# Optimization experiments

Measured on AMD Instinct MI355X. Metric: run time of the kernel, lower is better.

## Reference

```python
import jax, jax.numpy as jnp
import numpy as np

N_EMB = 1024
HEAD_SIZE = 128

def setup_inputs() -> dict:
    key = jax.random.key(0)
    kx, kq, kk, kv = jax.random.split(key, 4)
    s = 1.0 / np.sqrt(N_EMB)
    return {
        "x": jax.random.normal(kx, (4, 4096, N_EMB), dtype=jnp.float32),
        "Wq": jax.random.normal(kq, (N_EMB, HEAD_SIZE), dtype=jnp.float32) * s,
        "Wk": jax.random.normal(kk, (N_EMB, HEAD_SIZE), dtype=jnp.float32) * s,
        "Wv": jax.random.normal(kv, (N_EMB, HEAD_SIZE), dtype=jnp.float32) * s,
    }

def reference(x, Wq, Wk, Wv) -> jnp.ndarray:
    B, T, C = x.shape
    q = jnp.einsum('btc,cd->btd', x, Wq)  # [B,T,H]
    k = jnp.einsum('btc,cd->btd', x, Wk)
    v = jnp.einsum('btc,cd->btd', x, Wv)
    # NOTE: original scales by sqrt(n_emb), not sqrt(head_size)
    wei = jnp.einsum('btd,bsd->bts', q, k) / jnp.sqrt(jnp.asarray(C, x.dtype))
    causal = jnp.tril(jnp.ones((T, T), dtype=bool))
    wei = jnp.where(causal, wei, -jnp.inf)
    wei = jax.nn.softmax(wei, axis=-1)
    return jnp.einsum('bts,bsd->btd', wei, v)
```

## Files before the change

### kernel.cpp

```cpp
#include <hip/hip_runtime.h>
#include <hip/hip_bf16.h>


#define TSEQ 4096
#define NBATCH 4
#define CEMB 1024
#define HS 128
#define NWORK 144

typedef float  f32x4  __attribute__((ext_vector_type(4)));
typedef float  f32x16 __attribute__((ext_vector_type(16)));
typedef __bf16 bf16x4 __attribute__((ext_vector_type(4)));
typedef __bf16 bf16x8 __attribute__((ext_vector_type(8)));

__device__ __forceinline__ __bf16 f2b(float f) { return (__bf16)f; }
__device__ __forceinline__ float fexp2(float f) { return __builtin_amdgcn_exp2f(f); }

__global__ void wtrans_kernel(const float* __restrict__ Wq,
                              const float* __restrict__ Wk,
                              const float* __restrict__ Wv,
                              __bf16* __restrict__ Wt) {
  const float* W = (blockIdx.y == 0) ? Wq : (blockIdx.y == 1) ? Wk : Wv;
  int g  = blockIdx.x * 256 + threadIdx.x;
  int n  = g & 127;
  int k0 = (g >> 7) * 8;
  bf16x8 v;
#pragma unroll
  for (int i = 0; i < 8; ++i) v[i] = f2b(W[(size_t)(k0 + i) * HS + n]);
  *(bf16x8*)(Wt + (size_t)blockIdx.y * HS * CEMB + (size_t)n * CEMB + k0) = v;
}

__global__ __launch_bounds__(256)
void proj_kernel(const float* __restrict__ x, const __bf16* __restrict__ Wt,
                 __bf16* __restrict__ qb, __bf16* __restrict__ kb,
                 __bf16* __restrict__ vt) {
  __shared__ __align__(16) __bf16 As[32 * 64];
  __shared__ __align__(16) __bf16 Bs[128 * 64];

  const int tid  = threadIdx.x;
  const int lane = tid & 63;
  const int w    = tid >> 6;
  const int l31  = lane & 31;
  const int half = lane >> 5;

  const int bid = blockIdx.x;
  const int xcd = bid & 7;
  const int i3  = bid >> 3;
  const int mat = i3 % 3;
  const int mb  = xcd + 8 * (i3 / 3);
  const int m0  = mb * 32;
  const __bf16* Wm = Wt + (size_t)mat * HS * CEMB;

  f32x16 acc;
#pragma unroll
  for (int r = 0; r < 16; ++r) acc[r] = 0.f;

  const int ar = 8 * w + (lane >> 4);
  const int ac = lane & 15;
  const int br = 32 * w + (lane >> 3);
  const int bu = lane & 7;

  for (int ks = 0; ks < CEMB; ks += 64) {
    __syncthreads();
#pragma unroll
    for (int i = 0; i < 2; ++i) {
      int r = ar + 4 * i;
      f32x4 f = *(const f32x4*)(x + (size_t)(m0 + r) * CEMB + ks + ac * 4);
      bf16x4 h;
#pragma unroll
      for (int j = 0; j < 4; ++j) h[j] = f2b(f[j]);
      int u = ac >> 1;
      int up = u ^ (r & 7);
      *(bf16x4*)(As + r * 64 + up * 8 + (ac & 1) * 4) = h;
    }
#pragma unroll
    for (int i = 0; i < 4; ++i) {
      int r = br + 8 * i;
      bf16x8 v = *(const bf16x8*)(Wm + (size_t)r * CEMB + ks + bu * 8);
      int up = bu ^ (r & 7);
      *(bf16x8*)(Bs + r * 64 + up * 8) = v;
    }
    __syncthreads();
#pragma unroll
    for (int kc = 0; kc < 4; ++kc) {
      int ua = (2 * kc + half) ^ (l31 & 7);
      bf16x8 af = *(const bf16x8*)(As + l31 * 64 + ua * 8);
      bf16x8 bf = *(const bf16x8*)(Bs + (32 * w + l31) * 64 + ua * 8);
      acc = __builtin_amdgcn_mfma_f32_32x32x16_bf16(af, bf, acc, 0, 0, 0);
    }
  }

  const int n = 32 * w + l31;
  const float qscale = 1.4426950408889634f / 32.0f;
  if (mat == 0) {
#pragma unroll
    for (int r = 0; r < 16; ++r) {
      int m = m0 + (r & 3) + 8 * (r >> 2) + 4 * half;
      qb[(size_t)m * HS + n] = f2b(acc[r] * qscale);
    }
  } else if (mat == 1) {
#pragma unroll
    for (int r = 0; r < 16; ++r) {
      int m = m0 + (r & 3) + 8 * (r >> 2) + 4 * half;
      kb[(size_t)m * HS + n] = f2b(acc[r]);
    }
  } else {
    const int bt = mb >> 7;
#pragma unroll
    for (int g = 0; g < 4; ++g) {
      bf16x4 pk;
#pragma unroll
      for (int d = 0; d < 4; ++d) pk[d] = f2b(acc[4 * g + d]);
      int tl = (m0 & 4095) + 8 * g + 4 * half;
      *(bf16x4*)(vt + ((size_t)bt * HS + n) * TSEQ + tl) = pk;
    }
  }
}

__global__ __launch_bounds__(256)
void attn_kernel(const __bf16* __restrict__ qb, const __bf16* __restrict__ kb,
                 const __bf16* __restrict__ vt,
                 float* __restrict__ Opart, float* __restrict__ Lpart) {
  __shared__ __align__(16) __bf16 Kt[64 * 136];
  __shared__ __align__(16) __bf16 Vtl[128 * 72];
  __shared__ __align__(16) __bf16 Ptl[4 * 32 * 72];

  const int tid   = threadIdx.x;
  const int lane  = tid & 63;
  const int w     = tid >> 6;
  const int l31   = lane & 31;
  const int half  = lane >> 5;
  const int batch = blockIdx.y;
  const int xw    = NWORK - 1 - blockIdx.x;

  int g = 0;
  while (xw >= 2 * (g + 1) * (g + 2)) ++g;
  const int nsp   = g + 1;
  const int rel   = xw - 2 * g * (g + 1);
  const int qin   = rel / nsp;
  const int split = rel - qin * nsp;
  const int q     = 4 * g + qin;
  const int ntile = 2 * (q + 1);
  const int tps   = (ntile + nsp - 1) / nsp;
  const int it0   = split * tps;
  const int it1   = min(it0 + tps, ntile);

  const int strip0 = q * 128 + w * 32;
  const size_t bbase = (size_t)batch * TSEQ;

  bf16x8 qf[8];
  {
    const __bf16* qr = qb + (bbase + strip0 + l31) * HS + half * 8;
#pragma unroll
    for (int kc = 0; kc < 8; ++kc) qf[kc] = *(const bf16x8*)(qr + kc * 16);
  }

  f32x16 o[4];
#pragma unroll
  for (int nt = 0; nt < 4; ++nt)
#pragma unroll
    for (int r = 0; r < 16; ++r) o[nt][r] = 0.f;
  float lsum[16];
#pragma unroll
  for (int r = 0; r < 16; ++r) lsum[r] = 0.f;

  for (int it = it0; it < it1; ++it) {
    const int c0 = it * 64;
    __syncthreads();
    {
      const __bf16* src = kb + (bbase + c0) * HS;
#pragma unroll
      for (int i = 0; i < 4; ++i) {
        int c = tid + i * 256;
        int row = c >> 4, off = c & 15;
        *(int4*)(&Kt[row * 136 + off * 8]) = *(const int4*)(src + row * HS + off * 8);
      }
      const __bf16* vsrc = vt + (size_t)batch * HS * TSEQ + c0;
#pragma unroll
      for (int i = 0; i < 4; ++i) {
        int c = tid + i * 256;
        int n = c >> 3, off = c & 7;
        *(int4*)(&Vtl[n * 72 + off * 8]) = *(const int4*)(vsrc + (size_t)n * TSEQ + off * 8);
      }
    }
    __syncthreads();

    if (c0 <= strip0 + 31) {
      f32x16 s[2];
#pragma unroll
      for (int t = 0; t < 2; ++t)
#pragma unroll
        for (int r = 0; r < 16; ++r) s[t][r] = 0.f;
#pragma unroll
      for (int t = 0; t < 2; ++t)
#pragma unroll
        for (int kc = 0; kc < 8; ++kc) {
          bf16x8 kf = *(const bf16x8*)(&Kt[(t * 32 + l31) * 136 + kc * 16 + half * 8]);
          s[t] = __builtin_amdgcn_mfma_f32_32x32x16_bf16(qf[kc], kf, s[t], 0, 0, 0);
        }
#pragma unroll
      for (int t = 0; t < 2; ++t) {
        if (c0 + t * 32 + 31 > strip0) {
          int j = c0 + t * 32 + l31;
#pragma unroll
          for (int r = 0; r < 16; ++r) {
            int iloc = 4 * half + (r & 3) + 8 * (r >> 2);
            if (j > strip0 + iloc) s[t][r] = -INFINITY;
          }
        }
      }
#pragma unroll
      for (int r = 0; r < 16; ++r) {
        float p0 = fexp2(s[0][r]);
        float p1 = fexp2(s[1][r]);
        s[0][r] = p0; s[1][r] = p1;
        lsum[r] += p0 + p1;
      }
#pragma unroll
      for (int t = 0; t < 2; ++t)
#pragma unroll
        for (int r = 0; r < 16; ++r) {
          int iloc = 4 * half + (r & 3) + 8 * (r >> 2);
          Ptl[(w * 32 + iloc) * 72 + t * 32 + l31] = f2b(s[t][r]);
        }
      asm volatile("s_waitcnt lgkmcnt(0)" ::: "memory");
      bf16x8 pf[4];
#pragma unroll
      for (int kk = 0; kk < 4; ++kk)
        pf[kk] = *(const bf16x8*)(&Ptl[(w * 32 + l31) * 72 + kk * 16 + half * 8]);
#pragma unroll
      for (int nt = 0; nt < 4; ++nt)
#pragma unroll
        for (int kk = 0; kk < 4; ++kk) {
          bf16x8 vf = *(const bf16x8*)(&Vtl[(nt * 32 + l31) * 72 + kk * 16 + half * 8]);
          o[nt] = __builtin_amdgcn_mfma_f32_32x32x16_bf16(pf[kk], vf, o[nt], 0, 0, 0);
        }
    }
  }

  const size_t widx = (size_t)batch * NWORK + xw;
  float* Op = Opart + widx * (128 * 128);
#pragma unroll
  for (int r = 0; r < 16; ++r) {
    int rloc = w * 32 + 4 * half + (r & 3) + 8 * (r >> 2);
#pragma unroll
    for (int nt = 0; nt < 4; ++nt)
      Op[rloc * 128 + nt * 32 + l31] = o[nt][r];
  }
#pragma unroll
  for (int r = 0; r < 16; ++r) {
    float v = lsum[r];
    v += __shfl_xor(v, 1);
    v += __shfl_xor(v, 2);
    v += __shfl_xor(v, 4);
    v += __shfl_xor(v, 8);
    v += __shfl_xor(v, 16);
    lsum[r] = v;
  }
  if (l31 == 0) {
#pragma unroll
    for (int r = 0; r < 16; ++r) {
      int rloc = w * 32 + 4 * half + (r & 3) + 8 * (r >> 2);
      Lpart[widx * 128 + rloc] = lsum[r];
    }
  }
}

__global__ __launch_bounds__(256)
void reduce_kernel(const float* __restrict__ Opart, const float* __restrict__ Lpart,
                   float* __restrict__ out) {
  const int batch = blockIdx.y;
  const int rowg  = blockIdx.x * 8 + (threadIdx.x >> 5);
  const int q = rowg >> 7;
  const int g = q >> 2;
  const int nsp = g + 1;
  const int off = 2 * g * (g + 1) + (q & 3) * nsp;
  const size_t wbase = (size_t)batch * NWORK + off;
  const int row128 = rowg & 127;
  const int c0 = (threadIdx.x & 31) * 4;

  float l = 0.f;
  for (int s = 0; s < nsp; ++s) l += Lpart[(wbase + s) * 128 + row128];
  const float inv = 1.0f / l;

  const float* op = Opart + wbase * (128 * 128) + row128 * 128 + c0;
  f32x4 a = {0.f, 0.f, 0.f, 0.f};
  for (int s = 0; s < nsp; ++s)
    a += *(const f32x4*)(op + (size_t)s * 128 * 128);
  a *= inv;
  *(f32x4*)(out + ((size_t)batch * TSEQ + rowg) * HS + c0) = a;
}

extern "C" void kernel_launch(void* const* d_in, const int* in_sizes, int n_in,
                              void* d_out, int out_size, void* d_ws, size_t ws_size,
                              hipStream_t stream) {
  const float* x  = (const float*)d_in[0];
  const float* Wq = (const float*)d_in[1];
  const float* Wk = (const float*)d_in[2];
  const float* Wv = (const float*)d_in[3];
  float* out = (float*)d_out;

  char* ws = (char*)d_ws;
  __bf16* Wt = (__bf16*)ws;
  __bf16* qb = (__bf16*)(ws + 786432);
  __bf16* kb = (__bf16*)(ws + 786432 + 4194304);
  __bf16* vt = (__bf16*)(ws + 786432 + 2 * 4194304);
  float* Opart = (float*)(ws + 786432 + 3 * 4194304);
  float* Lpart = (float*)(ws + 786432 + 3 * 4194304 +
                          (size_t)NBATCH * NWORK * 128 * 128 * 4);

  wtrans_kernel<<<dim3(64, 3), 256, 0, stream>>>(Wq, Wk, Wv, Wt);
  proj_kernel<<<dim3(1536), 256, 0, stream>>>(x, Wt, qb, kb, vt);
  attn_kernel<<<dim3(NWORK, NBATCH), 256, 0, stream>>>(qb, kb, vt, Opart, Lpart);
  reduce_kernel<<<dim3(512, NBATCH), 256, 0, stream>>>(Opart, Lpart, out);
}
```

Before: 199.1 us.

## Rework attention kernel: transposed S, register P shuffle, async LDS loads, finer split

Computes S transposed (K as the A operand) so the probabilities land in the layout the PV MFMA needs, and exchanges them across half-waves with shuffles instead of a round trip through shared memory. K/V tiles are loaded straight into LDS with global_load_lds using an XOR swizzle in place of padding. The causal work split grows from 144 to 272 items per batch, and fully masked 32-key subtiles are skipped. Partial outputs are stored as bf16, halving reduce traffic but adding rounding error to the partial sums.

```diff
diff --git a/kernel.cpp b/kernel.cpp
--- a/kernel.cpp
+++ b/kernel.cpp
@@ -6,15 +6,23 @@
 #define NBATCH 4
 #define CEMB 1024
 #define HS 128
-#define NWORK 144
+#define NWORK 272
 
 typedef float  f32x4  __attribute__((ext_vector_type(4)));
 typedef float  f32x16 __attribute__((ext_vector_type(16)));
 typedef __bf16 bf16x4 __attribute__((ext_vector_type(4)));
 typedef __bf16 bf16x8 __attribute__((ext_vector_type(8)));
+typedef int    i32x2  __attribute__((ext_vector_type(2)));
+typedef int    i32x4  __attribute__((ext_vector_type(4)));
 
 __device__ __forceinline__ __bf16 f2b(float f) { return (__bf16)f; }
 __device__ __forceinline__ float fexp2(float f) { return __builtin_amdgcn_exp2f(f); }
+
+__device__ __forceinline__ void gl_lds16(const void* g, void* l) {
+  __builtin_amdgcn_global_load_lds(
+      (__attribute__((address_space(1))) void*)(g),
+      (__attribute__((address_space(3))) void*)(l), 16, 0, 0);
+}
 
 __global__ void wtrans_kernel(const float* __restrict__ Wq,
                               const float* __restrict__ Wk,
@@ -120,10 +128,9 @@
 __global__ __launch_bounds__(256)
 void attn_kernel(const __bf16* __restrict__ qb, const __bf16* __restrict__ kb,
                  const __bf16* __restrict__ vt,
-                 float* __restrict__ Opart, float* __restrict__ Lpart) {
-  __shared__ __align__(16) __bf16 Kt[64 * 136];
-  __shared__ __align__(16) __bf16 Vtl[128 * 72];
-  __shared__ __align__(16) __bf16 Ptl[4 * 32 * 72];
+                 __bf16* __restrict__ Opart, float* __restrict__ Lpart) {
+  __shared__ __align__(16) __bf16 Kt[64 * 128];
+  __shared__ __align__(16) __bf16 Vtl[128 * 64];
 
   const int tid   = threadIdx.x;
   const int lane  = tid & 63;
@@ -131,16 +138,13 @@
   const int l31   = lane & 31;
   const int half  = lane >> 5;
   const int batch = blockIdx.y;
-  const int xw    = NWORK - 1 - blockIdx.x;
-
-  int g = 0;
-  while (xw >= 2 * (g + 1) * (g + 2)) ++g;
-  const int nsp   = g + 1;
-  const int rel   = xw - 2 * g * (g + 1);
-  const int qin   = rel / nsp;
-  const int split = rel - qin * nsp;
-  const int q     = 4 * g + qin;
+  const int xw    = blockIdx.x;
+
+  int q = 0;
+  while (q < 31 && xw >= (((q + 2) * (q + 2)) >> 2)) ++q;
+  const int split = xw - (((q + 1) * (q + 1)) >> 2);
   const int ntile = 2 * (q + 1);
+  const int nsp   = (q + 2) >> 1;
   const int tps   = (ntile + nsp - 1) / nsp;
   const int it0   = split * tps;
   const int it1   = min(it0 + tps, ntile);
@@ -160,121 +164,113 @@
   for (int nt = 0; nt < 4; ++nt)
 #pragma unroll
     for (int r = 0; r < 16; ++r) o[nt][r] = 0.f;
-  float lsum[16];
-#pragma unroll
-  for (int r = 0; r < 16; ++r) lsum[r] = 0.f;
+  float lsum = 0.f;
 
   for (int it = it0; it < it1; ++it) {
     const int c0 = it * 64;
     __syncthreads();
-    {
-      const __bf16* src = kb + (bbase + c0) * HS;
-#pragma unroll
-      for (int i = 0; i < 4; ++i) {
-        int c = tid + i * 256;
-        int row = c >> 4, off = c & 15;
-        *(int4*)(&Kt[row * 136 + off * 8]) = *(const int4*)(src + row * HS + off * 8);
+#pragma unroll
+    for (int i = 0; i < 4; ++i) {
+      int ck = i * 4 + w;
+      {
+        int r  = 4 * ck + (lane >> 4);
+        int u1 = lane & 15;
+        int u  = (u1 & 8) | ((u1 & 7) ^ (r & 7));
+        gl_lds16(kb + (bbase + c0 + r) * HS + u * 8, &Kt[ck * 512]);
       }
-      const __bf16* vsrc = vt + (size_t)batch * HS * TSEQ + c0;
-#pragma unroll
-      for (int i = 0; i < 4; ++i) {
-        int c = tid + i * 256;
-        int n = c >> 3, off = c & 7;
-        *(int4*)(&Vtl[n * 72 + off * 8]) = *(const int4*)(vsrc + (size_t)n * TSEQ + off * 8);
+      {
+        int d  = 8 * ck + (lane >> 3);
+        int u1 = lane & 7;
+        int u  = u1 ^ (d & 7);
+        gl_lds16(vt + ((size_t)batch * HS + d) * TSEQ + c0 + u * 8, &Vtl[ck * 512]);
       }
     }
     __syncthreads();
 
     if (c0 <= strip0 + 31) {
-      f32x16 s[2];
+      i32x2 pkt[2][4];
 #pragma unroll
       for (int t = 0; t < 2; ++t)
 #pragma unroll
-        for (int r = 0; r < 16; ++r) s[t][r] = 0.f;
-#pragma unroll
-      for (int t = 0; t < 2; ++t)
-#pragma unroll
-        for (int kc = 0; kc < 8; ++kc) {
-          bf16x8 kf = *(const bf16x8*)(&Kt[(t * 32 + l31) * 136 + kc * 16 + half * 8]);
-          s[t] = __builtin_amdgcn_mfma_f32_32x32x16_bf16(qf[kc], kf, s[t], 0, 0, 0);
-        }
+        for (int j = 0; j < 4; ++j) pkt[t][j] = (i32x2){0, 0};
+
 #pragma unroll
       for (int t = 0; t < 2; ++t) {
-        if (c0 + t * 32 + 31 > strip0) {
-          int j = c0 + t * 32 + l31;
-#pragma unroll
-          for (int r = 0; r < 16; ++r) {
-            int iloc = 4 * half + (r & 3) + 8 * (r >> 2);
-            if (j > strip0 + iloc) s[t][r] = -INFINITY;
+        if (c0 + t * 32 <= strip0 + 31) {
+          f32x16 s;
+#pragma unroll
+          for (int r = 0; r < 16; ++r) s[r] = 0.f;
+#pragma unroll
+          for (int kc = 0; kc < 8; ++kc) {
+            int u  = 2 * kc + half;
+            int up = (u & 8) | ((u & 7) ^ (l31 & 7));
+            bf16x8 kf = *(const bf16x8*)(&Kt[(t * 32 + l31) * 128 + up * 8]);
+            s = __builtin_amdgcn_mfma_f32_32x32x16_bf16(kf, qf[kc], s, 0, 0, 0);
+          }
+          if (c0 + t * 32 + 31 > strip0) {
+#pragma unroll
+            for (int r = 0; r < 16; ++r) {
+              int key = c0 + t * 32 + (r & 3) + 8 * (r >> 2) + 4 * half;
+              if (key > strip0 + l31) s[r] = -INFINITY;
+            }
+          }
+          float p[16], ps = 0.f;
+#pragma unroll
+          for (int r = 0; r < 16; ++r) { p[r] = fexp2(s[r]); ps += p[r]; }
+          lsum += ps;
+#pragma unroll
+          for (int j = 0; j < 4; ++j) {
+            bf16x4 t4;
+#pragma unroll
+            for (int d = 0; d < 4; ++d) t4[d] = f2b(p[4 * j + d]);
+            pkt[t][j] = __builtin_bit_cast(i32x2, t4);
           }
         }
       }
 #pragma unroll
-      for (int r = 0; r < 16; ++r) {
-        float p0 = fexp2(s[0][r]);
-        float p1 = fexp2(s[1][r]);
-        s[0][r] = p0; s[1][r] = p1;
-        lsum[r] += p0 + p1;
+      for (int kk = 0; kk < 4; ++kk) {
+        int t = kk >> 1, lo = (kk & 1) * 2;
+        i32x2 a = pkt[t][lo], b = pkt[t][lo + 1];
+        i32x2 ra, rb;
+        ra.x = __shfl_xor(a.x, 32); ra.y = __shfl_xor(a.y, 32);
+        rb.x = __shfl_xor(b.x, 32); rb.y = __shfl_xor(b.y, 32);
+        i32x4 af4;
+        af4.x = half ? rb.x : a.x;
+        af4.y = half ? rb.y : a.y;
+        af4.z = half ? b.x  : ra.x;
+        af4.w = half ? b.y  : ra.y;
+        bf16x8 af = __builtin_bit_cast(bf16x8, af4);
+#pragma unroll
+        for (int nt = 0; nt < 4; ++nt) {
+          int up = (2 * kk + half) ^ (l31 & 7);
+          bf16x8 vf = *(const bf16x8*)(&Vtl[(nt * 32 + l31) * 64 + up * 8]);
+          o[nt] = __builtin_amdgcn_mfma_f32_32x32x16_bf16(af, vf, o[nt], 0, 0, 0);
+        }
       }
-#pragma unroll
-      for (int t = 0; t < 2; ++t)
-#pragma unroll
-        for (int r = 0; r < 16; ++r) {
-          int iloc = 4 * half + (r & 3) + 8 * (r >> 2);
-          Ptl[(w * 32 + iloc) * 72 + t * 32 + l31] = f2b(s[t][r]);
-        }
-      asm volatile("s_waitcnt lgkmcnt(0)" ::: "memory");
-      bf16x8 pf[4];
-#pragma unroll
-      for (int kk = 0; kk < 4; ++kk)
-        pf[kk] = *(const bf16x8*)(&Ptl[(w * 32 + l31) * 72 + kk * 16 + half * 8]);
-#pragma unroll
-      for (int nt = 0; nt < 4; ++nt)
-#pragma unroll
-        for (int kk = 0; kk < 4; ++kk) {
-          bf16x8 vf = *(const bf16x8*)(&Vtl[(nt * 32 + l31) * 72 + kk * 16 + half * 8]);
-          o[nt] = __builtin_amdgcn_mfma_f32_32x32x16_bf16(pf[kk], vf, o[nt], 0, 0, 0);
-        }
     }
   }
 
   const size_t widx = (size_t)batch * NWORK + xw;
-  float* Op = Opart + widx * (128 * 128);
+  __bf16* Op = Opart + widx * (128 * 128);
 #pragma unroll
   for (int r = 0; r < 16; ++r) {
     int rloc = w * 32 + 4 * half + (r & 3) + 8 * (r >> 2);
 #pragma unroll
     for (int nt = 0; nt < 4; ++nt)
-      Op[rloc * 128 + nt * 32 + l31] = o[nt][r];
-  }
-#pragma unroll
-  for (int r = 0; r < 16; ++r) {
-    float v = lsum[r];
-    v += __shfl_xor(v, 1);
-    v += __shfl_xor(v, 2);
-    v += __shfl_xor(v, 4);
-    v += __shfl_xor(v, 8);
-    v += __shfl_xor(v, 16);
-    lsum[r] = v;
-  }
-  if (l31 == 0) {
-#pragma unroll
-    for (int r = 0; r < 16; ++r) {
-      int rloc = w * 32 + 4 * half + (r & 3) + 8 * (r >> 2);
-      Lpart[widx * 128 + rloc] = lsum[r];
-    }
-  }
+      Op[rloc * 128 + nt * 32 + l31] = f2b(o[nt][r]);
+  }
+  lsum += __shfl_xor(lsum, 32);
+  if (half == 0) Lpart[widx * 128 + w * 32 + l31] = lsum;
 }
 
 __global__ __launch_bounds__(256)
-void reduce_kernel(const float* __restrict__ Opart, const float* __restrict__ Lpart,
+void reduce_kernel(const __bf16* __restrict__ Opart, const float* __restrict__ Lpart,
                    float* __restrict__ out) {
   const int batch = blockIdx.y;
   const int rowg  = blockIdx.x * 8 + (threadIdx.x >> 5);
   const int q = rowg >> 7;
-  const int g = q >> 2;
-  const int nsp = g + 1;
-  const int off = 2 * g * (g + 1) + (q & 3) * nsp;
+  const int nsp = (q + 2) >> 1;
+  const int off = ((q + 1) * (q + 1)) >> 2;
   const size_t wbase = (size_t)batch * NWORK + off;
   const int row128 = rowg & 127;
   const int c0 = (threadIdx.x & 31) * 4;
@@ -283,10 +279,13 @@
   for (int s = 0; s < nsp; ++s) l += Lpart[(wbase + s) * 128 + row128];
   const float inv = 1.0f / l;
 
-  const float* op = Opart + wbase * (128 * 128) + row128 * 128 + c0;
+  const __bf16* op = Opart + wbase * (128 * 128) + row128 * 128 + c0;
   f32x4 a = {0.f, 0.f, 0.f, 0.f};
-  for (int s = 0; s < nsp; ++s)
-    a += *(const f32x4*)(op + (size_t)s * 128 * 128);
+  for (int s = 0; s < nsp; ++s) {
+    bf16x4 v = *(const bf16x4*)(op + (size_t)s * 128 * 128);
+#pragma unroll
+    for (int j = 0; j < 4; ++j) a[j] += (float)v[j];
+  }
   a *= inv;
   *(f32x4*)(out + ((size_t)batch * TSEQ + rowg) * HS + c0) = a;
 }
@@ -305,9 +304,9 @@
   __bf16* qb = (__bf16*)(ws + 786432);
   __bf16* kb = (__bf16*)(ws + 786432 + 4194304);
   __bf16* vt = (__bf16*)(ws + 786432 + 2 * 4194304);
-  float* Opart = (float*)(ws + 786432 + 3 * 4194304);
-  float* Lpart = (float*)(ws + 786432 + 3 * 4194304 +
-                          (size_t)NBATCH * NWORK * 128 * 128 * 4);
+  __bf16* Opart = (__bf16*)(ws + 786432 + 3 * 4194304);
+  float*  Lpart = (float*)(ws + 786432 + 3 * 4194304 +
+                           (size_t)NBATCH * NWORK * 128 * 128 * 2);
 
   wtrans_kernel<<<dim3(64, 3), 256, 0, stream>>>(Wq, Wk, Wv, Wt);
   proj_kernel<<<dim3(1536), 256, 0, stream>>>(x, Wt, qb, kb, vt);
```

Result: faster. 182.1 us (-8.6%).
